# Kernel tuning notes

Measured on AMD Instinct MI355X. Metric: run time of the kernel, lower is better.

The kernel has to match this reference:

```python
import jax, jax.numpy as jnp
import numpy as np

NUM_HEADS = 16


def setup_inputs() -> dict:
    key = jax.random.key(0)
    ks = jax.random.split(key, 6)
    B, S, H = 4, 2048, 1024
    x = jax.random.normal(ks[0], (B, S, H), dtype=jnp.float32)
    mask = jax.random.randint(ks[1], (B, 1, 1, S), 0, 2, dtype=jnp.int32)
    scale = 1.0 / np.sqrt(H)
    Wq = jax.random.normal(ks[2], (H, H), dtype=jnp.float32) * scale
    Wk = jax.random.normal(ks[3], (H, H), dtype=jnp.float32) * scale
    Wv = jax.random.normal(ks[4], (H, H), dtype=jnp.float32) * scale
    Wo = jax.random.normal(ks[5], (H, H), dtype=jnp.float32) * scale
    bo = jnp.zeros((H,), dtype=jnp.float32)
    return {"x": x, "mask": mask, "Wq": Wq, "Wk": Wk, "Wv": Wv, "Wo": Wo, "bo": bo}


def reference(x, mask, Wq, Wk, Wv, Wo, bo):
    B, S, H = x.shape
    nh = NUM_HEADS
    dk = H // nh

    def split_heads(t):  # (B,S,H) -> (B,nh,S,dk)
        return t.reshape(B, S, nh, dk).transpose(0, 2, 1, 3)

    # torch Linear: y = x @ W.T (q/k/v bias-free)
    q = split_heads(x @ Wq.T)
    k = split_heads(x @ Wk.T)
    v = split_heads(x @ Wv.T)

    scores = jnp.einsum('bhqd,bhkd->bhqk', q, k) / jnp.sqrt(jnp.float32(dk))
    scores = jnp.where(mask == 0, jnp.float32(-1e9), scores)
    attn = jax.nn.softmax(scores, axis=-1)  # dropout is identity in eval mode
    out = jnp.einsum('bhqk,bhkd->bhqd', attn, v)
    out = out.transpose(0, 2, 1, 3).reshape(B, S, H)
    return out @ Wo.T + bo
```

## Files before the change

kernel.cpp:

```cpp
#include <hip/hip_runtime.h>
#include <hip/hip_bf16.h>

typedef __attribute__((ext_vector_type(8))) short sh8;
typedef __attribute__((ext_vector_type(4))) float f32x4;

#define MFMA16(a, b, c) __builtin_amdgcn_mfma_f32_16x16x32_bf16((a), (b), (c), 0, 0, 0)

__device__ __forceinline__ unsigned short f2bf(float f) {
    return (unsigned short)((__float_as_uint(f) + 0x8000u) >> 16);
}
__device__ __forceinline__ unsigned int pack2bf(float lo, float hi) {
    unsigned int ul = __float_as_uint(lo) + 0x8000u;
    unsigned int uh = __float_as_uint(hi) + 0x8000u;
    return __builtin_amdgcn_perm(uh, ul, 0x07060302u);
}
__device__ __forceinline__ float redmax_hi(float x) {
    x = fmaxf(x, __shfl_xor(x, 16, 64));
    return fmaxf(x, __shfl_xor(x, 32, 64));
}
__device__ __forceinline__ float redsum_hi(float x) {
    x += __shfl_xor(x, 16, 64);
    return x + __shfl_xor(x, 32, 64);
}

__global__ __launch_bounds__(64) void compact_k(
    const int* __restrict__ mask, int* __restrict__ idx, int* __restrict__ cnt)
{
    const int b = blockIdx.x, l = threadIdx.x;
    const int* mb = mask + b * 2048;
    int base = 0;
    for (int i = 0; i < 32; ++i) {
        int m = mb[i * 64 + l];
        unsigned long long bal = __ballot(m != 0);
        int pre = __popcll(bal & ((1ull << l) - 1ull));
        if (m) idx[b * 2048 + base + pre] = i * 64 + l;
        base += (int)__popcll(bal);
    }
    if (base == 0) {
        for (int i = l; i < 2048; i += 64) idx[b * 2048 + i] = i;
        base = 2048;
    }
    if (l == 0) cnt[b] = base;
}

__global__ __launch_bounds__(256) void gemm_qkv_k(
    const float* __restrict__ x, const float* __restrict__ Wq,
    const float* __restrict__ Wk, const float* __restrict__ Wv,
    unsigned short* __restrict__ qkv)
{
    __shared__ unsigned short As[128][48];
    __shared__ unsigned short Bs[128][48];
    const int tid = threadIdx.x;
    const int l = tid & 63, w = tid >> 6;
    const int wr = w >> 1, wc = w & 1;
    const long row0 = (long)blockIdx.y * 128;
    const int col0 = blockIdx.x * 128;
    const float* Wsel; int wrow0;
    if (col0 < 1024)      { Wsel = Wq; wrow0 = col0; }
    else if (col0 < 2048) { Wsel = Wk; wrow0 = col0 - 1024; }
    else                  { Wsel = Wv; wrow0 = col0 - 2048; }

    f32x4 acc[4][4] = {};
    const int fr = l & 15, fc = (l >> 4) * 8;

    for (int k0 = 0; k0 < 1024; k0 += 32) {
        __syncthreads();
#pragma unroll
        for (int p = 0; p < 4; ++p) {
            int idx_ = p * 256 + tid;
            int r = idx_ >> 3, c4 = (idx_ & 7) * 4;
            float4 va = *(const float4*)&x[(row0 + r) * 1024 + k0 + c4];
            uint2 ha = { pack2bf(va.x, va.y), pack2bf(va.z, va.w) };
            *(uint2*)&As[r][c4] = ha;
            float4 vb = *(const float4*)&Wsel[(long)(wrow0 + r) * 1024 + k0 + c4];
            uint2 hb = { pack2bf(vb.x, vb.y), pack2bf(vb.z, vb.w) };
            *(uint2*)&Bs[r][c4] = hb;
        }
        __syncthreads();
        sh8 af[4], bf[4];
#pragma unroll
        for (int i = 0; i < 4; ++i) {
            af[i] = *(const sh8*)&As[wr * 64 + i * 16 + fr][fc];
            bf[i] = *(const sh8*)&Bs[wc * 64 + i * 16 + fr][fc];
        }
#pragma unroll
        for (int i = 0; i < 4; ++i)
#pragma unroll
            for (int j = 0; j < 4; ++j)
                acc[i][j] = MFMA16(af[i], bf[j], acc[i][j]);
    }

    const float scale = (col0 < 1024) ? 0.1803368801f : 1.0f;
    const int rg = (l >> 4) * 4, cg = l & 15;
#pragma unroll
    for (int i = 0; i < 4; ++i)
#pragma unroll
        for (int j = 0; j < 4; ++j) {
            long gr = row0 + wr * 64 + i * 16 + rg;
            int gc = col0 + wc * 64 + j * 16 + cg;
#pragma unroll
            for (int r = 0; r < 4; ++r)
                qkv[(gr + r) * 3072 + gc] = f2bf(acc[i][j][r] * scale);
        }
}

__global__ __launch_bounds__(256) void attn_k(
    const unsigned short* __restrict__ qkv, const int* __restrict__ idx,
    const int* __restrict__ cnt, unsigned short* __restrict__ ao, int b0)
{
    __shared__ unsigned short Kl[64][64];
    __shared__ unsigned short Vt[64][64];
    __shared__ float biasf[64];
    __shared__ unsigned short Pl[4][16][72];

    const int tid = threadIdx.x;
    const int l = tid & 63, w = tid >> 6;
    const int fr = l & 15, hi = l >> 4;

    int nwg = gridDim.x;
    int wgid = ((nwg & 7) == 0) ? ((blockIdx.x & 7) * (nwg >> 3) + (blockIdx.x >> 3))
                                : blockIdx.x;
    const int qb = wgid & 15;
    const int h  = (wgid >> 4) & 15;
    const int b  = wgid >> 8;
    const int q0 = qb * 128;
    const long base = (long)b * 2048;

    const int* idxb = idx + (size_t)(b0 + b) * 2048;
    const int nc = cnt[b0 + b];
    const int nt = (nc + 63) >> 6;

    sh8 qf[2][2];
#pragma unroll
    for (int g = 0; g < 2; ++g) {
        const unsigned short* qp = &qkv[(base + q0 + w * 32 + g * 16 + fr) * 3072 + h * 64 + hi * 8];
        qf[g][0] = *(const sh8*)qp;
        qf[g][1] = *(const sh8*)(qp + 32);
    }

    f32x4 acc[2][4] = {};
    float mrow[2] = { -1e30f, -1e30f };
    float lrow[2] = { 0.f, 0.f };

    const int rK = tid >> 3, cc = tid & 7;
    const int kv2 = tid >> 3, dc = tid & 7;

    uint4 k0r, k1r, v0r, v1r;
    {
        int ik0 = idxb[min(rK, nc - 1)];
        int ik1 = idxb[min(rK + 32, nc - 1)];
        int iv0 = idxb[min(2 * kv2, nc - 1)];
        int iv1 = idxb[min(2 * kv2 + 1, nc - 1)];
        k0r = *(const uint4*)&qkv[(base + ik0) * 3072 + 1024 + h * 64 + cc * 8];
        k1r = *(const uint4*)&qkv[(base + ik1) * 3072 + 1024 + h * 64 + cc * 8];
        v0r = *(const uint4*)&qkv[(base + iv0) * 3072 + 2048 + h * 64 + dc * 8];
        v1r = *(const uint4*)&qkv[(base + iv1) * 3072 + 2048 + h * 64 + dc * 8];
    }

    for (int t = 0; t < nt; ++t) {
        __syncthreads();
        *(uint4*)&Kl[rK][(cc ^ (rK & 7)) * 8] = k0r;
        {
            int r2 = rK + 32;
            *(uint4*)&Kl[r2][(cc ^ (r2 & 7)) * 8] = k1r;
        }
        {
            unsigned int w0[4] = { v0r.x, v0r.y, v0r.z, v0r.w };
            unsigned int w1[4] = { v1r.x, v1r.y, v1r.z, v1r.w };
            int cc2 = kv2 >> 2, pos = (2 * kv2) & 7;
#pragma unroll
            for (int jj = 0; jj < 4; ++jj) {
                int de = dc * 8 + 2 * jj;
                unsigned int pe = (w0[jj] & 0xffffu) | (w1[jj] << 16);
                unsigned int po = (w0[jj] >> 16) | (w1[jj] & 0xffff0000u);
                int fde = (2 * jj) ^ dc;
                int fdo = (2 * jj + 1) ^ dc;
                *(unsigned int*)&Vt[de][((cc2 ^ fde) * 8) + pos] = pe;
                *(unsigned int*)&Vt[de + 1][((cc2 ^ fdo) * 8) + pos] = po;
            }
        }
        if (tid < 64) biasf[tid] = (t * 64 + tid < nc) ? 0.0f : -1e9f;
        __syncthreads();

        if (t + 1 < nt) {
            int s0 = (t + 1) * 64;
            int ik0 = idxb[min(s0 + rK, nc - 1)];
            int ik1 = idxb[min(s0 + rK + 32, nc - 1)];
            int iv0 = idxb[min(s0 + 2 * kv2, nc - 1)];
            int iv1 = idxb[min(s0 + 2 * kv2 + 1, nc - 1)];
            k0r = *(const uint4*)&qkv[(base + ik0) * 3072 + 1024 + h * 64 + cc * 8];
            k1r = *(const uint4*)&qkv[(base + ik1) * 3072 + 1024 + h * 64 + cc * 8];
            v0r = *(const uint4*)&qkv[(base + iv0) * 3072 + 2048 + h * 64 + dc * 8];
            v1r = *(const uint4*)&qkv[(base + iv1) * 3072 + 2048 + h * 64 + dc * 8];
        }

        sh8 kf[4][2];
#pragma unroll
        for (int tt = 0; tt < 4; ++tt) {
            const unsigned short* kp = &Kl[tt * 16 + fr][0];
#pragma unroll
            for (int c = 0; c < 2; ++c)
                kf[tt][c] = *(const sh8*)&kp[((4 * c + hi) ^ (fr & 7)) * 8];
        }

#pragma unroll
        for (int g = 0; g < 2; ++g) {
            f32x4 s[4] = {};
            __builtin_amdgcn_s_setprio(1);
#pragma unroll
            for (int tt = 0; tt < 4; ++tt) {
                s[tt] = MFMA16(kf[tt][0], qf[g][0], s[tt]);
                s[tt] = MFMA16(kf[tt][1], qf[g][1], s[tt]);
            }
            __builtin_amdgcn_s_setprio(0);
#pragma unroll
            for (int tt = 0; tt < 4; ++tt)
                s[tt] += *(const f32x4*)&biasf[tt * 16 + 4 * hi];

            float pm = s[0][0];
#pragma unroll
            for (int tt = 0; tt < 4; ++tt)
#pragma unroll
                for (int r = 0; r < 4; ++r) pm = fmaxf(pm, s[tt][r]);
            pm = redmax_hi(pm);

            float mr = mrow[g];
            if (!__all(pm <= mr)) {
                float mn = fmaxf(mr, pm);
                float scl = __builtin_amdgcn_exp2f(mr - mn);
                lrow[g] *= scl;
#pragma unroll
                for (int df = 0; df < 4; ++df) acc[g][df] *= scl;
                mrow[g] = mn;
                mr = mn;
            }

            float ps = 0.f;
#pragma unroll
            for (int tt = 0; tt < 4; ++tt)
#pragma unroll
                for (int r = 0; r < 4; ++r) {
                    float p = __builtin_amdgcn_exp2f(s[tt][r] - mr);
                    s[tt][r] = p;
                    ps += p;
                }
            lrow[g] += redsum_hi(ps);

#pragma unroll
            for (int tt = 0; tt < 4; ++tt) {
                uint2 pw = { pack2bf(s[tt][0], s[tt][1]), pack2bf(s[tt][2], s[tt][3]) };
                *(uint2*)&Pl[w][fr][tt * 16 + hi * 4] = pw;
            }

#pragma unroll
            for (int c = 0; c < 2; ++c) {
                sh8 pa = *(const sh8*)&Pl[w][fr][c * 32 + hi * 8];
                __builtin_amdgcn_s_setprio(1);
#pragma unroll
                for (int df = 0; df < 4; ++df) {
                    int d = df * 16 + fr;
                    int fd = (d & 7) ^ (d >> 3);
                    sh8 vfr = *(const sh8*)&Vt[d][((4 * c + hi) ^ fd) * 8];
                    acc[g][df] = MFMA16(vfr, pa, acc[g][df]);
                }
                __builtin_amdgcn_s_setprio(0);
            }
        }
    }

#pragma unroll
    for (int g = 0; g < 2; ++g) {
        float inv = 1.0f / lrow[g];
        long qr = base + q0 + w * 32 + g * 16 + fr;
        unsigned short* op = &ao[qr * 1024 + h * 64];
#pragma unroll
        for (int df = 0; df < 4; ++df) {
            f32x4 o = acc[g][df];
            uint2 ow = { pack2bf(o[0] * inv, o[1] * inv), pack2bf(o[2] * inv, o[3] * inv) };
            *(uint2*)&op[df * 16 + hi * 4] = ow;
        }
    }
}

__global__ __launch_bounds__(256) void gemm_out_k(
    const unsigned short* __restrict__ ao, const float* __restrict__ Wo,
    const float* __restrict__ bo, float* __restrict__ out)
{
    __shared__ unsigned short As[128][48];
    __shared__ unsigned short Bs[128][48];
    const int tid = threadIdx.x;
    const int l = tid & 63, w = tid >> 6;
    const int wr = w >> 1, wc = w & 1;
    const long row0 = (long)blockIdx.y * 128;
    const int col0 = blockIdx.x * 128;

    f32x4 acc[4][4] = {};
    const int fr = l & 15, fc = (l >> 4) * 8;

    for (int k0 = 0; k0 < 1024; k0 += 32) {
        __syncthreads();
#pragma unroll
        for (int p = 0; p < 2; ++p) {
            int idx_ = p * 256 + tid;
            int r = idx_ >> 2, c8 = (idx_ & 3) * 8;
            uint4 v = *(const uint4*)&ao[(row0 + r) * 1024 + k0 + c8];
            *(uint2*)&As[r][c8] = make_uint2(v.x, v.y);
            *(uint2*)&As[r][c8 + 4] = make_uint2(v.z, v.w);
        }
#pragma unroll
        for (int p = 0; p < 4; ++p) {
            int idx_ = p * 256 + tid;
            int r = idx_ >> 3, c4 = (idx_ & 7) * 4;
            float4 vb = *(const float4*)&Wo[(long)(col0 + r) * 1024 + k0 + c4];
            uint2 hb = { pack2bf(vb.x, vb.y), pack2bf(vb.z, vb.w) };
            *(uint2*)&Bs[r][c4] = hb;
        }
        __syncthreads();
        sh8 af[4], bf[4];
#pragma unroll
        for (int i = 0; i < 4; ++i) {
            af[i] = *(const sh8*)&As[wr * 64 + i * 16 + fr][fc];
            bf[i] = *(const sh8*)&Bs[wc * 64 + i * 16 + fr][fc];
        }
#pragma unroll
        for (int i = 0; i < 4; ++i)
#pragma unroll
            for (int j = 0; j < 4; ++j)
                acc[i][j] = MFMA16(af[i], bf[j], acc[i][j]);
    }

    const int rg = (l >> 4) * 4, cg = l & 15;
#pragma unroll
    for (int i = 0; i < 4; ++i)
#pragma unroll
        for (int j = 0; j < 4; ++j) {
            long gr = row0 + wr * 64 + i * 16 + rg;
            int gc = col0 + wc * 64 + j * 16 + cg;
            float bb = bo[gc];
#pragma unroll
            for (int r = 0; r < 4; ++r)
                out[(gr + r) * 1024 + gc] = acc[i][j][r] + bb;
        }
}

extern "C" void kernel_launch(void* const* d_in, const int* in_sizes, int n_in,
                              void* d_out, int out_size, void* d_ws, size_t ws_size,
                              hipStream_t stream) {
    const float* x    = (const float*)d_in[0];
    const int*   mask = (const int*)d_in[1];
    const float* Wq   = (const float*)d_in[2];
    const float* Wk   = (const float*)d_in[3];
    const float* Wv   = (const float*)d_in[4];
    const float* Wo   = (const float*)d_in[5];
    const float* bo   = (const float*)d_in[6];
    float* out = (float*)d_out;

    const size_t qkv_per_b = (size_t)2048 * 3072 * 2;
    const size_t ao_per_b  = (size_t)2048 * 1024 * 2;
    const size_t per_b = qkv_per_b + ao_per_b;
    const size_t idx_bytes = (size_t)4 * 2048 * 4 + 4 * 4;
    size_t avail = (ws_size > idx_bytes) ? (ws_size - idx_bytes) : 0;
    int bchunk = (avail >= per_b) ? (int)(avail / per_b) : 1;
    if (bchunk > 4) bchunk = 4;

    unsigned short* qkv = (unsigned short*)d_ws;
    unsigned short* ao  = (unsigned short*)((char*)d_ws + (size_t)bchunk * qkv_per_b);
    int* idxp = (int*)((char*)d_ws + (size_t)bchunk * per_b);
    int* cntp = idxp + 4 * 2048;

    compact_k<<<4, 64, 0, stream>>>(mask, idxp, cntp);

    for (int b0 = 0; b0 < 4; b0 += bchunk) {
        int bc = (4 - b0 < bchunk) ? (4 - b0) : bchunk;
        gemm_qkv_k<<<dim3(24, bc * 16), 256, 0, stream>>>(
            x + (size_t)b0 * 2048 * 1024, Wq, Wk, Wv, qkv);
        attn_k<<<dim3(256 * bc), 256, 0, stream>>>(qkv, idxp, cntp, ao, b0);
        gemm_out_k<<<dim3(8, bc * 16), 256, 0, stream>>>(
            ao, Wo, bo, out + (size_t)b0 * 2048 * 1024);
    }
}
```

Measured before the change: 237.2 us.

## Pre-convert x and weights to bf16 and stage GEMM tiles via direct global-to-LDS loads

Adds separate kernels that convert x and the four weight matrices to bf16 once per call. The QKV and output GEMMs then fetch bf16 tiles with global_load_lds, writing straight into unpadded shared memory instead of loading fp32, converting and storing through registers. This halves GEMM operand traffic and removes repeated conversion work inside the tile loop. The cost is extra conversion passes, a larger workspace, and possible LDS bank conflicts since the padding is gone.

```diff
diff --git a/kernel.cpp b/kernel.cpp
--- a/kernel.cpp
+++ b/kernel.cpp
@@ -21,6 +21,36 @@
 __device__ __forceinline__ float redsum_hi(float x) {
     x += __shfl_xor(x, 16, 64);
     return x + __shfl_xor(x, 32, 64);
+}
+__device__ __forceinline__ void gload_lds16(const void* g, void* l) {
+    __builtin_amdgcn_global_load_lds(
+        (const __attribute__((address_space(1))) unsigned int*)g,
+        (__attribute__((address_space(3))) unsigned int*)l, 16, 0, 0);
+}
+
+__global__ __launch_bounds__(256) void cvt_x_k(
+    const float* __restrict__ src, unsigned short* __restrict__ dst, int n4)
+{
+    int i = blockIdx.x * 256 + threadIdx.x;
+    int stride = gridDim.x * 256;
+    for (; i < n4; i += stride) {
+        float4 v = ((const float4*)src)[i];
+        uint2 h = { pack2bf(v.x, v.y), pack2bf(v.z, v.w) };
+        ((uint2*)dst)[i] = h;
+    }
+}
+__global__ __launch_bounds__(256) void cvt_w_k(
+    const float* __restrict__ Wq, const float* __restrict__ Wk,
+    const float* __restrict__ Wv, const float* __restrict__ Wo,
+    unsigned short* __restrict__ wbf)
+{
+    int i = blockIdx.x * 256 + threadIdx.x;
+    int seg = i >> 18;
+    int off = i & 0x3FFFF;
+    const float* s = (seg < 2) ? ((seg == 0) ? Wq : Wk) : ((seg == 2) ? Wv : Wo);
+    float4 v = ((const float4*)s)[off];
+    uint2 h = { pack2bf(v.x, v.y), pack2bf(v.z, v.w) };
+    ((uint2*)wbf)[i] = h;
 }
 
 __global__ __launch_bounds__(64) void compact_k(
@@ -44,44 +74,41 @@
 }
 
 __global__ __launch_bounds__(256) void gemm_qkv_k(
-    const float* __restrict__ x, const float* __restrict__ Wq,
-    const float* __restrict__ Wk, const float* __restrict__ Wv,
+    const unsigned short* __restrict__ xbf,
+    const unsigned short* __restrict__ wbf,
     unsigned short* __restrict__ qkv)
 {
-    __shared__ unsigned short As[128][48];
-    __shared__ unsigned short Bs[128][48];
+    __shared__ unsigned short As[128][32];
+    __shared__ unsigned short Bs[128][32];
     const int tid = threadIdx.x;
     const int l = tid & 63, w = tid >> 6;
     const int wr = w >> 1, wc = w & 1;
     const long row0 = (long)blockIdx.y * 128;
     const int col0 = blockIdx.x * 128;
-    const float* Wsel; int wrow0;
-    if (col0 < 1024)      { Wsel = Wq; wrow0 = col0; }
-    else if (col0 < 2048) { Wsel = Wk; wrow0 = col0 - 1024; }
-    else                  { Wsel = Wv; wrow0 = col0 - 2048; }
 
     f32x4 acc[4][4] = {};
-    const int fr = l & 15, fc = (l >> 4) * 8;
+    const int fr = l & 15, hi = l >> 4;
+
+    const int sr = tid >> 2;
+    const int sc = (tid & 3) * 8;
+    const unsigned short* ga = &xbf[(row0 + sr) * 1024 + sc];
+    const unsigned short* gb = &wbf[(long)(col0 + sr) * 1024 + sc];
+    unsigned short* la = &As[w * 16][0];
+    unsigned short* lb = &Bs[w * 16][0];
 
     for (int k0 = 0; k0 < 1024; k0 += 32) {
         __syncthreads();
-#pragma unroll
-        for (int p = 0; p < 4; ++p) {
-            int idx_ = p * 256 + tid;
-            int r = idx_ >> 3, c4 = (idx_ & 7) * 4;
-            float4 va = *(const float4*)&x[(row0 + r) * 1024 + k0 + c4];
-            uint2 ha = { pack2bf(va.x, va.y), pack2bf(va.z, va.w) };
-            *(uint2*)&As[r][c4] = ha;
-            float4 vb = *(const float4*)&Wsel[(long)(wrow0 + r) * 1024 + k0 + c4];
-            uint2 hb = { pack2bf(vb.x, vb.y), pack2bf(vb.z, vb.w) };
-            *(uint2*)&Bs[r][c4] = hb;
-        }
-        __syncthreads();
+        gload_lds16(ga + k0, la);
+        gload_lds16(ga + 64 * 1024 + k0, la + 64 * 32);
+        gload_lds16(gb + k0, lb);
+        gload_lds16(gb + 64 * 1024 + k0, lb + 64 * 32);
+        __syncthreads();
+
         sh8 af[4], bf[4];
 #pragma unroll
         for (int i = 0; i < 4; ++i) {
-            af[i] = *(const sh8*)&As[wr * 64 + i * 16 + fr][fc];
-            bf[i] = *(const sh8*)&Bs[wc * 64 + i * 16 + fr][fc];
+            af[i] = *(const sh8*)&As[wr * 64 + i * 16 + fr][hi * 8];
+            bf[i] = *(const sh8*)&Bs[wc * 64 + i * 16 + fr][hi * 8];
         }
 #pragma unroll
         for (int i = 0; i < 4; ++i)
@@ -91,7 +118,7 @@
     }
 
     const float scale = (col0 < 1024) ? 0.1803368801f : 1.0f;
-    const int rg = (l >> 4) * 4, cg = l & 15;
+    const int rg = hi * 4, cg = l & 15;
 #pragma unroll
     for (int i = 0; i < 4; ++i)
 #pragma unroll
@@ -283,11 +310,11 @@
 }
 
 __global__ __launch_bounds__(256) void gemm_out_k(
-    const unsigned short* __restrict__ ao, const float* __restrict__ Wo,
+    const unsigned short* __restrict__ ao, const unsigned short* __restrict__ wob,
     const float* __restrict__ bo, float* __restrict__ out)
 {
-    __shared__ unsigned short As[128][48];
-    __shared__ unsigned short Bs[128][48];
+    __shared__ unsigned short As[128][32];
+    __shared__ unsigned short Bs[128][32];
     const int tid = threadIdx.x;
     const int l = tid & 63, w = tid >> 6;
     const int wr = w >> 1, wc = w & 1;
@@ -295,32 +322,28 @@
     const int col0 = blockIdx.x * 128;
 
     f32x4 acc[4][4] = {};
-    const int fr = l & 15, fc = (l >> 4) * 8;
+    const int fr = l & 15, hi = l >> 4;
+
+    const int sr = tid >> 2;
+    const int sc = (tid & 3) * 8;
+    const unsigned short* ga = &ao[(row0 + sr) * 1024 + sc];
+    const unsigned short* gb = &wob[(long)(col0 + sr) * 1024 + sc];
+    unsigned short* la = &As[w * 16][0];
+    unsigned short* lb = &Bs[w * 16][0];
 
     for (int k0 = 0; k0 < 1024; k0 += 32) {
         __syncthreads();
-#pragma unroll
-        for (int p = 0; p < 2; ++p) {
-            int idx_ = p * 256 + tid;
-            int r = idx_ >> 2, c8 = (idx_ & 3) * 8;
-            uint4 v = *(const uint4*)&ao[(row0 + r) * 1024 + k0 + c8];
-            *(uint2*)&As[r][c8] = make_uint2(v.x, v.y);
-            *(uint2*)&As[r][c8 + 4] = make_uint2(v.z, v.w);
-        }
-#pragma unroll
-        for (int p = 0; p < 4; ++p) {
-            int idx_ = p * 256 + tid;
-            int r = idx_ >> 3, c4 = (idx_ & 7) * 4;
-            float4 vb = *(const float4*)&Wo[(long)(col0 + r) * 1024 + k0 + c4];
-            uint2 hb = { pack2bf(vb.x, vb.y), pack2bf(vb.z, vb.w) };
-            *(uint2*)&Bs[r][c4] = hb;
-        }
-        __syncthreads();
+        gload_lds16(ga + k0, la);
+        gload_lds16(ga + 64 * 1024 + k0, la + 64 * 32);
+        gload_lds16(gb + k0, lb);
+        gload_lds16(gb + 64 * 1024 + k0, lb + 64 * 32);
+        __syncthreads();
+
         sh8 af[4], bf[4];
 #pragma unroll
         for (int i = 0; i < 4; ++i) {
-            af[i] = *(const sh8*)&As[wr * 64 + i * 16 + fr][fc];
-            bf[i] = *(const sh8*)&Bs[wc * 64 + i * 16 + fr][fc];
+            af[i] = *(const sh8*)&As[wr * 64 + i * 16 + fr][hi * 8];
+            bf[i] = *(const sh8*)&Bs[wc * 64 + i * 16 + fr][hi * 8];
         }
 #pragma unroll
         for (int i = 0; i < 4; ++i)
@@ -329,7 +352,7 @@
                 acc[i][j] = MFMA16(af[i], bf[j], acc[i][j]);
     }
 
-    const int rg = (l >> 4) * 4, cg = l & 15;
+    const int rg = hi * 4, cg = l & 15;
 #pragma unroll
     for (int i = 0; i < 4; ++i)
 #pragma unroll
@@ -355,27 +378,36 @@
     const float* bo   = (const float*)d_in[6];
     float* out = (float*)d_out;
 
+    const size_t wbf_bytes = (size_t)4096 * 1024 * 2;
+    const size_t idx_bytes = (size_t)4 * 2048 * 4 + 64;
+    const size_t xbf_per_b = (size_t)2048 * 1024 * 2;
     const size_t qkv_per_b = (size_t)2048 * 3072 * 2;
     const size_t ao_per_b  = (size_t)2048 * 1024 * 2;
-    const size_t per_b = qkv_per_b + ao_per_b;
-    const size_t idx_bytes = (size_t)4 * 2048 * 4 + 4 * 4;
-    size_t avail = (ws_size > idx_bytes) ? (ws_size - idx_bytes) : 0;
+    const size_t per_b = xbf_per_b + qkv_per_b + ao_per_b;
+
+    size_t fixed = wbf_bytes + idx_bytes;
+    size_t avail = (ws_size > fixed) ? (ws_size - fixed) : 0;
     int bchunk = (avail >= per_b) ? (int)(avail / per_b) : 1;
     if (bchunk > 4) bchunk = 4;
 
-    unsigned short* qkv = (unsigned short*)d_ws;
-    unsigned short* ao  = (unsigned short*)((char*)d_ws + (size_t)bchunk * qkv_per_b);
-    int* idxp = (int*)((char*)d_ws + (size_t)bchunk * per_b);
-    int* cntp = idxp + 4 * 2048;
-
+    char* p = (char*)d_ws;
+    unsigned short* wbf = (unsigned short*)p;            p += wbf_bytes;
+    int* idxp = (int*)p;                                 p += (size_t)4 * 2048 * 4;
+    int* cntp = (int*)p;                                 p += 64;
+    unsigned short* xbf = (unsigned short*)p;            p += (size_t)bchunk * xbf_per_b;
+    unsigned short* qkv = (unsigned short*)p;            p += (size_t)bchunk * qkv_per_b;
+    unsigned short* ao  = (unsigned short*)p;
+
+    cvt_w_k<<<4096, 256, 0, stream>>>(Wq, Wk, Wv, Wo, wbf);
     compact_k<<<4, 64, 0, stream>>>(mask, idxp, cntp);
 
     for (int b0 = 0; b0 < 4; b0 += bchunk) {
         int bc = (4 - b0 < bchunk) ? (4 - b0) : bchunk;
-        gemm_qkv_k<<<dim3(24, bc * 16), 256, 0, stream>>>(
-            x + (size_t)b0 * 2048 * 1024, Wq, Wk, Wv, qkv);
+        cvt_x_k<<<2048, 256, 0, stream>>>(
+            x + (size_t)b0 * 2048 * 1024, xbf, bc * 524288);
+        gemm_qkv_k<<<dim3(24, bc * 16), 256, 0, stream>>>(xbf, wbf, qkv);
         attn_k<<<dim3(256 * bc), 256, 0, stream>>>(qkv, idxp, cntp, ao, b0);
         gemm_out_k<<<dim3(8, bc * 16), 256, 0, stream>>>(
-            ao, Wo, bo, out + (size_t)b0 * 2048 * 1024);
-    }
-}
+            ao, wbf + (size_t)3072 * 1024, bo, out + (size_t)b0 * 2048 * 1024);
+    }
+}
```

Result: faster. 214.5 us (-9.6%).
